# Kernel tuning notes

Measured on AMD Instinct MI355X. Metric: run time of the kernel, lower is better.

Reference implementation:

```python
import jax, jax.numpy as jnp
import numpy as np

DIM = 512; HEADS = 8; DH = 64; CHUNK = 64; DHID = DH * 4; MAX_LR = 1.0; EPS = 1e-6


def rmsnorm(x, w):
    return x * jax.lax.rsqrt(jnp.mean(x * x, axis=-1, keepdims=True) + EPS) * w


def mem_forward(params, x):
    # MemoryMLP(depth=2, expansion=4) wrapped in ResidualNorm
    nw, w0, w1 = params
    h = rmsnorm(x, nw)
    y = jax.nn.gelu(h @ w0) @ w1
    return y + x


def chunk_loss(params, k, lr, v):
    pred = mem_forward(params, k)            # (CHUNK, DH)
    loss = jnp.mean((pred - v) ** 2, axis=-1)  # per-token mse, (CHUNK,)
    return (loss * lr).sum(), loss


def assoc_scan(gates, inputs, prev=None):
    # h_t = g_t * h_{t-1} + x_t along axis=1 (chunks)
    def combine(a, b):
        g1, x1 = a; g2, x2 = b
        return g1 * g2, x2 + g2 * x1
    G, X = jax.lax.associative_scan(combine, (gates, inputs), axis=1)
    if prev is None:
        return X
    return X + G * prev[:, None]


def setup_inputs() -> dict:
    key = jax.random.key(0)
    ks = jax.random.split(key, 8)
    B, N = 2, 4096
    s = 0.02
    return {
        'seq': jax.random.normal(ks[0], (B, N, DIM), jnp.float32),
        'store_norm_w': jnp.ones((DIM,), jnp.float32),
        'Wk': jax.random.normal(ks[1], (DIM, HEADS * DH), jnp.float32) * s,
        'Wv': jax.random.normal(ks[2], (DIM, HEADS * DH), jnp.float32) * s,
        'Wstep': jax.random.normal(ks[3], (DIM, HEADS), jnp.float32) * s,
        'bstep': jnp.zeros((HEADS,), jnp.float32),
        'Wmom': jax.random.normal(ks[4], (DIM, HEADS), jnp.float32) * s,
        'bmom': jnp.zeros((HEADS,), jnp.float32),
        'Wdec': jax.random.normal(ks[5], (DIM, HEADS), jnp.float32) * s,
        'bdec': jnp.zeros((HEADS,), jnp.float32),
        'mem_norm_w': jnp.ones((HEADS, DH), jnp.float32),
        'mem_w0': jax.random.normal(ks[6], (HEADS, DH, DHID), jnp.float32) * s,
        'mem_w1': jax.random.normal(ks[7], (HEADS, DHID, DH), jnp.float32) * s,
    }


def reference(seq, store_norm_w, Wk, Wv, Wstep, bstep, Wmom, bmom, Wdec, bdec, mem_norm_w, mem_w0, mem_w1):
    B, N, _ = seq.shape
    nc = N // CHUNK
    bh = B * HEADS
    x = rmsnorm(seq, store_norm_w)                        # store pre-norm, (B,N,D)
    # per-token adaptive lr: 'b n h -> (b h) n', sigmoid * max_lr
    lr = jax.nn.sigmoid(x @ Wstep + bstep) * MAX_LR       # (B,N,H)
    lr = lr.transpose(0, 2, 1).reshape(bh, nc, CHUNK)
    # chunk-pooled rep (AveragePool) -> momentum / decay gates per chunk
    pooled = x.reshape(B, nc, CHUNK, DIM).mean(axis=2)    # (B,nc,D)
    mom = jax.nn.sigmoid(pooled @ Wmom + bmom).transpose(0, 2, 1).reshape(bh, nc, 1)
    decay = jax.nn.sigmoid(pooled @ Wdec + bdec).transpose(0, 2, 1).reshape(bh, nc, 1)

    def split(t):  # (B,N,H*DH) -> (bh, nc, CHUNK, DH)
        return t.reshape(B, N, HEADS, DH).transpose(0, 2, 1, 3).reshape(bh, nc, CHUNK, DH)
    k = split(x @ Wk)
    v = split(x @ Wv)

    # initial fast weights per (b h) stream: repeat 'h ... -> (b h) ...'
    params0 = (jnp.tile(mem_norm_w, (B, 1)),
               jnp.tile(mem_w0, (B, 1, 1)),
               jnp.tile(mem_w1, (B, 1, 1)))

    # per-chunk per-stream grads via vmap(grad) (all chunks share the initial weights)
    grad_fn = jax.grad(chunk_loss, has_aux=True)
    per_chunk = jax.vmap(grad_fn, in_axes=(None, 0, 0, 0))
    per_bh = jax.vmap(per_chunk, in_axes=(0, 0, 0, 0))
    grads, _ = per_bh(params0, k, lr, v)                  # tuple of (bh, nc, *shape)

    finals = []
    for g, w0 in zip(grads, params0):
        surprise = -g
        extra = (1,) * (g.ndim - 2)
        m = mom.reshape(bh, nc, *extra)
        d = decay.reshape(bh, nc, *extra)
        update = assoc_scan(m, surprise)                  # momentum scan, zero init
        wts = assoc_scan(1.0 - d, update, prev=w0)        # decay recurrence from init weights
        finals.append(wts[:, -1].reshape(bh, -1))
    return jnp.concatenate(finals, axis=-1)              # (bh, DH + DH*DHID + DHID*DH)
```

## Files before the change

kernel.cpp:

```cpp
#include <hip/hip_runtime.h>
#include <math.h>

typedef __attribute__((ext_vector_type(8)))  __bf16 bf16x8;
typedef __attribute__((ext_vector_type(4)))  float  f32x4;
typedef __attribute__((ext_vector_type(4)))  unsigned short ushort4v;
typedef __attribute__((ext_vector_type(8)))  unsigned short ushort8v;

#define MFMA16(acc, a, b) acc = __builtin_amdgcn_mfma_f32_16x16x32_bf16((a),(b),(acc),0,0,0)

__device__ inline unsigned short f2b(float f) {
    __bf16 b = (__bf16)f;
    union { __bf16 b; unsigned short u; } v; v.b = b;
    return v.u;
}
__device__ inline float b2f(unsigned short h) {
    union { unsigned int u; float f; } v; v.u = ((unsigned int)h) << 16;
    return v.f;
}
__device__ inline float fast_rcp(float x) { return __builtin_amdgcn_rcpf(x); }
__device__ inline float tanh_fast(float z) {
    float e = __expf(2.0f * z);
    return 1.0f - 2.0f * fast_rcp(e + 1.0f);
}
__device__ inline float gelu_g(float x) {
    const float c0 = 0.7978845608028654f, c1 = 0.044715f;
    float z = c0 * x * (1.0f + c1 * x * x);
    return 0.5f * x * (1.0f + tanh_fast(z));
}
__device__ inline void gelu_both(float x, float& g, float& gp) {
    const float c0 = 0.7978845608028654f, c1 = 0.044715f;
    float x2 = x * x;
    float z  = c0 * x * (1.0f + c1 * x2);
    float t  = tanh_fast(z);
    g  = 0.5f * x * (1.0f + t);
    float dz = c0 * (1.0f + 3.0f * c1 * x2);
    gp = 0.5f * (1.0f + t) + 0.5f * x * (1.0f - t * t) * dz;
}
__device__ inline float sigmoidf(float x) { return fast_rcp(1.0f + __expf(-x)); }

__global__ __launch_bounds__(256) void k_wprep(
    const float* __restrict__ Wk, const float* __restrict__ Wv,
    const float* __restrict__ w0_g, const float* __restrict__ w1_g,
    const float* __restrict__ nw_g,
    unsigned short* __restrict__ WkvT, unsigned short* __restrict__ w0fT,
    unsigned short* __restrict__ w1T, unsigned short* __restrict__ w0N,
    unsigned short* __restrict__ w1N)
{
    const int bid = blockIdx.x, tid = threadIdx.x;
    __shared__ float tile[64][65];
    if (bid < 128) {
        int kt = bid >> 4, nt = bid & 15;
        const float* src = (nt < 8) ? Wk : Wv;
        int ncol0 = (nt & 7) * 64;
        for (int ii = 0; ii < 16; ++ii) {
            int idx = tid + ii * 256; int r = idx >> 6, cc = idx & 63;
            tile[r][cc] = src[(size_t)(kt * 64 + r) * 512 + ncol0 + cc];
        }
        __syncthreads();
        for (int ii = 0; ii < 16; ++ii) {
            int idx = tid + ii * 256; int r = idx >> 6, cc = idx & 63;
            WkvT[(size_t)(nt * 64 + r) * 512 + kt * 64 + cc] = f2b(tile[cc][r]);
        }
    } else if (bid < 160) {
        int q = bid - 128; int hh = q >> 2, it = q & 3;
        const float* w0h = w0_g + hh * 16384;
        for (int ii = 0; ii < 16; ++ii) {
            int idx = tid + ii * 256; int r = idx >> 6, cc = idx & 63;
            tile[r][cc] = w0h[r * 256 + it * 64 + cc];
        }
        __syncthreads();
        for (int ii = 0; ii < 16; ++ii) {
            int idx = tid + ii * 256; int r = idx >> 6, cc = idx & 63;
            w0fT[hh * 16384 + (it * 64 + r) * 64 + cc] = f2b(nw_g[hh * 64 + cc] * tile[cc][r]);
        }
    } else if (bid < 192) {
        int q = bid - 160; int hh = q >> 2, it = q & 3;
        const float* w1h = w1_g + hh * 16384;
        for (int ii = 0; ii < 16; ++ii) {
            int idx = tid + ii * 256; int r = idx >> 6, cc = idx & 63;
            tile[r][cc] = w1h[(it * 64 + r) * 64 + cc];
        }
        __syncthreads();
        for (int ii = 0; ii < 16; ++ii) {
            int idx = tid + ii * 256; int r = idx >> 6, cc = idx & 63;
            w1T[hh * 16384 + r * 256 + it * 64 + cc] = f2b(tile[cc][r]);
        }
    } else {
        int q = bid - 192;
        int gid = q * 2048 + tid * 8;
        const float* s; unsigned short* d;
        if (gid < 131072) { s = w0_g + gid; d = w0N + gid; }
        else              { s = w1_g + (gid - 131072); d = w1N + (gid - 131072); }
        #pragma unroll
        for (int jj = 0; jj < 8; ++jj) d[jj] = f2b(s[jj]);
    }
}

__global__ __launch_bounds__(256) void k_rms_lr(
    const float* __restrict__ seq, const float* __restrict__ wnorm,
    const float* __restrict__ Wstep, const float* __restrict__ bstep,
    unsigned short* __restrict__ xb, float* __restrict__ lrb)
{
    const int wid = threadIdx.x >> 6, lane = threadIdx.x & 63;
    const int t = blockIdx.x * 4 + wid;
    const float* row = seq + (size_t)t * 512 + lane * 8;
    float v[8];
    *(f32x4*)&v[0] = *(const f32x4*)row;
    *(f32x4*)&v[4] = *(const f32x4*)(row + 4);
    float ss = 0.f;
    #pragma unroll
    for (int j = 0; j < 8; ++j) ss += v[j] * v[j];
    #pragma unroll
    for (int o = 1; o < 64; o <<= 1) ss += __shfl_xor(ss, o);
    float rr = rsqrtf(ss * (1.0f / 512.0f) + 1e-6f);
    const float* wn = wnorm + lane * 8;
    ushort8v xs;
    float acc[8] = {0.f,0.f,0.f,0.f,0.f,0.f,0.f,0.f};
    #pragma unroll
    for (int j = 0; j < 8; ++j) {
        float xf = v[j] * rr * wn[j];
        xs[j] = f2b(xf);
        const float* wrow = Wstep + (size_t)(lane * 8 + j) * 8;
        #pragma unroll
        for (int h = 0; h < 8; ++h) acc[h] = fmaf(xf, wrow[h], acc[h]);
    }
    *(ushort8v*)(xb + (size_t)t * 512 + lane * 8) = xs;
    #pragma unroll
    for (int h = 0; h < 8; ++h) {
        #pragma unroll
        for (int o = 1; o < 64; o <<= 1) acc[h] += __shfl_xor(acc[h], o);
    }
    if (lane == 0) {
        #pragma unroll
        for (int h = 0; h < 8; ++h) lrb[(size_t)t * 8 + h] = sigmoidf(acc[h] + bstep[h]);
    }
}

__global__ __launch_bounds__(256) void k_poolgates(
    const unsigned short* __restrict__ xb,
    const float* __restrict__ Wmom, const float* __restrict__ bmom,
    const float* __restrict__ Wdec, const float* __restrict__ bdec,
    float* __restrict__ momout, float* __restrict__ decout)
{
    __shared__ float sP[4][512];
    __shared__ float pooled[512];
    const int bc = blockIdx.x, tid = threadIdx.x;
    const int q = tid >> 6, lane = tid & 63, d0 = lane * 8;
    float p[8] = {0.f,0.f,0.f,0.f,0.f,0.f,0.f,0.f};
    for (int tt = 0; tt < 16; ++tt) {
        int t = q * 16 + tt;
        ushort8v v = *(const ushort8v*)(xb + (size_t)(bc * 64 + t) * 512 + d0);
        #pragma unroll
        for (int j = 0; j < 8; ++j) p[j] += b2f(v[j]);
    }
    #pragma unroll
    for (int j = 0; j < 8; ++j) sP[q][d0 + j] = p[j];
    __syncthreads();
    #pragma unroll
    for (int half = 0; half < 2; ++half) {
        int d = tid + half * 256;
        pooled[d] = (sP[0][d] + sP[1][d] + sP[2][d] + sP[3][d]) * (1.0f / 64.0f);
    }
    __syncthreads();
    if (tid < 64) {
        const int h = tid & 7, dd0 = tid >> 3;
        float pm = 0.f, pd = 0.f;
        #pragma unroll 8
        for (int it = 0; it < 64; ++it) {
            int d = dd0 + it * 8; float pv = pooled[d];
            pm = fmaf(pv, Wmom[d * 8 + h], pm);
            pd = fmaf(pv, Wdec[d * 8 + h], pd);
        }
        #pragma unroll
        for (int o = 8; o < 64; o <<= 1) { pm += __shfl_xor(pm, o); pd += __shfl_xor(pd, o); }
        if (tid < 8) {
            momout[(size_t)bc * 8 + h] = sigmoidf(pm + bmom[h]);
            decout[(size_t)bc * 8 + h] = sigmoidf(pd + bdec[h]);
        }
    }
}

__global__ __launch_bounds__(256) void k_proj(
    const unsigned short* __restrict__ xb, const unsigned short* __restrict__ WkvT,
    unsigned short* __restrict__ kbh, unsigned short* __restrict__ vb)
{
    __shared__ __attribute__((aligned(16))) unsigned short As[128][72];
    __shared__ __attribute__((aligned(16))) unsigned short Bs[128][72];
    const int tid = threadIdx.x;
    const int bm = blockIdx.x >> 3, bn = blockIdx.x & 7;
    const int m0 = bm * 128, n0 = bn * 128;
    const int wid = tid >> 6, lane = tid & 63, lg = lane >> 4, lo = lane & 15;
    const int wm = wid >> 1, wn = wid & 1;
    f32x4 acc[4][4];
    #pragma unroll
    for (int i = 0; i < 4; ++i)
        #pragma unroll
        for (int j = 0; j < 4; ++j) acc[i][j] = (f32x4)0.f;

    for (int k0 = 0; k0 < 512; k0 += 64) {
        #pragma unroll
        for (int ii = 0; ii < 4; ++ii) {
            int e0 = tid * 32 + ii * 8;
            int r = e0 >> 6, c = e0 & 63;
            *(bf16x8*)&As[r][c] = *(const bf16x8*)(xb   + (size_t)(m0 + r) * 512 + k0 + c);
            *(bf16x8*)&Bs[r][c] = *(const bf16x8*)(WkvT + (size_t)(n0 + r) * 512 + k0 + c);
        }
        __syncthreads();
        #pragma unroll
        for (int ks = 0; ks < 2; ++ks) {
            bf16x8 aF[4], bF[4];
            #pragma unroll
            for (int mt = 0; mt < 4; ++mt) aF[mt] = *(const bf16x8*)&As[wm * 64 + mt * 16 + lo][ks * 32 + 8 * lg];
            #pragma unroll
            for (int nt = 0; nt < 4; ++nt) bF[nt] = *(const bf16x8*)&Bs[wn * 64 + nt * 16 + lo][ks * 32 + 8 * lg];
            #pragma unroll
            for (int mt = 0; mt < 4; ++mt)
                #pragma unroll
                for (int nt = 0; nt < 4; ++nt) MFMA16(acc[mt][nt], aF[mt], bF[nt]);
        }
        __syncthreads();
    }
    #pragma unroll
    for (int mt = 0; mt < 4; ++mt)
        #pragma unroll
        for (int nt = 0; nt < 4; ++nt)
            #pragma unroll
            for (int r = 0; r < 4; ++r) {
                int row = m0 + wm * 64 + mt * 16 + lg * 4 + r;
                int col = n0 + wn * 64 + nt * 16 + lo;
                unsigned short val = f2b(acc[mt][nt][r]);
                if (col < 512) kbh[(size_t)row * 512 + col] = val;
                else           vb[(size_t)row * 512 + col - 512] = val;
            }
}

__global__ void k_coeff(const float* __restrict__ mom, const float* __restrict__ dec,
                        float* __restrict__ coeff, float* __restrict__ Aout)
{
    __shared__ float sm[1024], sd[1024];
    int tid = threadIdx.x;
    #pragma unroll
    for (int i = 0; i < 4; ++i) {
        int idx = (tid + i * 64) * 4;
        *(f32x4*)&sm[idx] = *(const f32x4*)&mom[idx];
        *(f32x4*)&sd[idx] = *(const f32x4*)&dec[idx];
    }
    __syncthreads();
    int s = tid;
    if (s >= 16) return;
    int b = s >> 3, h = s & 7;
    float P = 1.f, S = 1.f;
    coeff[s * 64 + 63] = 1.f;
    for (int cc = 62; cc >= 0; --cc) {
        float Dn = 1.f - sd[(b * 64 + cc + 1) * 8 + h];
        float Mn = sm[(b * 64 + cc + 1) * 8 + h];
        P *= Dn;
        S = P + Mn * S;
        coeff[s * 64 + cc] = S;
    }
    float D0 = 1.f - sd[(b * 64) * 8 + h];
    Aout[s] = P * D0;
}

__global__ __launch_bounds__(256) void k_fwd(
    const unsigned short* __restrict__ kbh, const unsigned short* __restrict__ vb,
    const float* __restrict__ lrb, const float* __restrict__ cfb,
    const unsigned short* __restrict__ w0fT, const unsigned short* __restrict__ w1T,
    unsigned short* __restrict__ uws, unsigned short* __restrict__ ews,
    unsigned short* __restrict__ ewsT)
{
    __shared__ __attribute__((aligned(16))) unsigned short sU[64][72];
    __shared__ __attribute__((aligned(16))) unsigned short sG[2][64][72];
    const int tid = threadIdx.x, blk = blockIdx.x;
    const int s = blk >> 6, c = blk & 63;
    const int b = s >> 3, h = s & 7;
    const int row0 = b * 4096 + c * 64;
    const int wid = tid >> 6, lane = tid & 63, lg = lane >> 4, lo = lane & 15;
    const size_t ubase = (size_t)blk * 4096;

    {
        int r = tid >> 2, c0 = (tid & 3) * 16;
        const unsigned short* kr = kbh + (size_t)(row0 + r) * 512 + h * 64 + c0;
        ushort8v k0 = *(const ushort8v*)kr;
        ushort8v k1 = *(const ushort8v*)(kr + 8);
        float kv[16];
        float ss = 0.f;
        #pragma unroll
        for (int j = 0; j < 8; ++j) { kv[j] = b2f(k0[j]); kv[8 + j] = b2f(k1[j]); }
        #pragma unroll
        for (int j = 0; j < 16; ++j) ss += kv[j] * kv[j];
        ss += __shfl_xor(ss, 1);
        ss += __shfl_xor(ss, 2);
        float rr = rsqrtf(ss * (1.0f / 64.0f) + 1e-6f);
        ushort8v u0, u1;
        #pragma unroll
        for (int j = 0; j < 8; ++j) { u0[j] = f2b(kv[j] * rr); u1[j] = f2b(kv[8 + j] * rr); }
        *(ushort8v*)&sU[r][c0]     = u0;
        *(ushort8v*)&sU[r][c0 + 8] = u1;
        *(ushort8v*)(uws + ubase + r * 64 + c0)     = u0;
        *(ushort8v*)(uws + ubase + r * 64 + c0 + 8) = u1;
    }
    __syncthreads();

    const unsigned short* w0h = w0fT + h * 16384;
    const unsigned short* w1h = w1T  + h * 16384;
    bf16x8 aF0 = *(const bf16x8*)&sU[wid * 16 + lo][8 * lg];
    bf16x8 aF1 = *(const bf16x8*)&sU[wid * 16 + lo][32 + 8 * lg];

    f32x4 yac[4];
    #pragma unroll
    for (int nt = 0; nt < 4; ++nt) yac[nt] = (f32x4)0.f;

    for (int is = 0; is < 4; ++is) {
        const int bi = is & 1;
        f32x4 a1[4];
        #pragma unroll
        for (int nt = 0; nt < 4; ++nt) a1[nt] = (f32x4)0.f;
        #pragma unroll
        for (int nt = 0; nt < 4; ++nt) {
            bf16x8 b0 = *(const bf16x8*)(w0h + (size_t)(is * 64 + nt * 16 + lo) * 64 + 8 * lg);
            bf16x8 b1 = *(const bf16x8*)(w0h + (size_t)(is * 64 + nt * 16 + lo) * 64 + 32 + 8 * lg);
            MFMA16(a1[nt], aF0, b0);
            MFMA16(a1[nt], aF1, b1);
        }
        #pragma unroll
        for (int nt = 0; nt < 4; ++nt)
            #pragma unroll
            for (int r = 0; r < 4; ++r) {
                int t = wid * 16 + lg * 4 + r;
                sG[bi][t][nt * 16 + lo] = f2b(gelu_g(a1[nt][r]));
            }
        __syncthreads();
        #pragma unroll
        for (int ks = 0; ks < 2; ++ks) {
            bf16x8 aW = *(const bf16x8*)(w1h + (size_t)(wid * 16 + lo) * 256 + is * 64 + ks * 32 + 8 * lg);
            #pragma unroll
            for (int nt = 0; nt < 4; ++nt) {
                bf16x8 bG = *(const bf16x8*)&sG[bi][nt * 16 + lo][ks * 32 + 8 * lg];
                MFMA16(yac[nt], aW, bG);
            }
        }
    }

    float coefv = cfb[s * 64 + c];
    ushort4v evs[4];
    #pragma unroll
    for (int nt = 0; nt < 4; ++nt) {
        int t = nt * 16 + lo; int grow = row0 + t;
        float sc = -coefv * lrb[(size_t)grow * 8 + h] * (2.0f / 64.0f);
        ushort4v k4 = *(const ushort4v*)(kbh + (size_t)grow * 512 + h * 64 + wid * 16 + lg * 4);
        ushort4v v4 = *(const ushort4v*)(vb  + (size_t)grow * 512 + h * 64 + wid * 16 + lg * 4);
        ushort4v ev;
        #pragma unroll
        for (int r = 0; r < 4; ++r)
            ev[r] = f2b(sc * (yac[nt][r] + b2f(k4[r]) - b2f(v4[r])));
        evs[nt] = ev;
        *(ushort4v*)(ews + ubase + t * 64 + wid * 16 + lg * 4) = ev;
    }

    #pragma unroll
    for (int nt = 0; nt < 4; ++nt)
        *(ushort4v*)&sG[0][nt * 16 + lo][wid * 16 + lg * 4] = evs[nt];
    __syncthreads();
    {
        int r2 = tid >> 2, c2 = (tid & 3) * 16;
        ushort8v o0, o1;
        #pragma unroll
        for (int jj = 0; jj < 8; ++jj) o0[jj] = sG[0][c2 + jj][r2];
        #pragma unroll
        for (int jj = 0; jj < 8; ++jj) o1[jj] = sG[0][c2 + 8 + jj][r2];
        *(ushort8v*)(ewsT + ubase + r2 * 64 + c2)     = o0;
        *(ushort8v*)(ewsT + ubase + r2 * 64 + c2 + 8) = o1;
    }
}

__global__ __launch_bounds__(256) void k_bwd(
    const unsigned short* __restrict__ uws, const unsigned short* __restrict__ ews,
    const unsigned short* __restrict__ ewsT,
    const unsigned short* __restrict__ w0fT, const unsigned short* __restrict__ w0N,
    const unsigned short* __restrict__ w1N, const float* __restrict__ nw_g,
    float* __restrict__ pws, float* __restrict__ gnwb)
{
    __shared__ __attribute__((aligned(16))) unsigned short sGT[2][64][72];
    __shared__ __attribute__((aligned(16))) unsigned short sDAT[2][64][72];
    __shared__ __attribute__((aligned(16))) unsigned short sDAN[2][64][68];
    const int tid = threadIdx.x, blk = blockIdx.x;
    const int s = blk >> 5, ksl = (blk >> 2) & 7, is = blk & 3;
    const int h = s & 7;
    const int wid = tid >> 6, lane = tid & 63, lg = lane >> 4, lo = lane & 15;

    f32x4 gw1a[4], gw0a[4];
    #pragma unroll
    for (int nt = 0; nt < 4; ++nt) { gw1a[nt] = (f32x4)0.f; gw0a[nt] = (f32x4)0.f; }
    float gnwp[4] = {0.f, 0.f, 0.f, 0.f};

    const unsigned short* w0fh = w0fT + h * 16384;
    const unsigned short* w0nh = w0N  + h * 16384;
    const unsigned short* w1nh = w1N  + h * 16384;

    for (int tt = 0; tt < 8; ++tt) {
        const int bi = tt & 1;
        const int chunk = ksl * 8 + tt;
        const size_t base = (size_t)(s * 64 + chunk) * 4096;

        unsigned short utg[16];
        #pragma unroll
        for (int ks = 0; ks < 2; ++ks)
            #pragma unroll
            for (int jj = 0; jj < 8; ++jj)
                utg[ks * 8 + jj] = uws[base + (size_t)(ks * 32 + 8 * lg + jj) * 64 + wid * 16 + lo];
        ushort4v u4n[4];
        #pragma unroll
        for (int nt = 0; nt < 4; ++nt)
            u4n[nt] = *(const ushort4v*)(uws + base + (size_t)(nt * 16 + lo) * 64 + wid * 16 + lg * 4);

        f32x4 a1[4];
        #pragma unroll
        for (int nt = 0; nt < 4; ++nt) a1[nt] = (f32x4)0.f;
        bf16x8 aF0 = *(const bf16x8*)(uws + base + (size_t)(wid * 16 + lo) * 64 + 8 * lg);
        bf16x8 aF1 = *(const bf16x8*)(uws + base + (size_t)(wid * 16 + lo) * 64 + 32 + 8 * lg);
        #pragma unroll
        for (int nt = 0; nt < 4; ++nt) {
            bf16x8 b0 = *(const bf16x8*)(w0fh + (size_t)(is * 64 + nt * 16 + lo) * 64 + 8 * lg);
            bf16x8 b1 = *(const bf16x8*)(w0fh + (size_t)(is * 64 + nt * 16 + lo) * 64 + 32 + 8 * lg);
            MFMA16(a1[nt], aF0, b0);
            MFMA16(a1[nt], aF1, b1);
        }
        float gpv[4][4];
        #pragma unroll
        for (int nt = 0; nt < 4; ++nt) {
            ushort4v gv;
            #pragma unroll
            for (int r = 0; r < 4; ++r) {
                float g, gp; gelu_both(a1[nt][r], g, gp);
                gv[r] = f2b(g); gpv[nt][r] = gp;
            }
            *(ushort4v*)&sGT[bi][nt * 16 + lo][wid * 16 + lg * 4] = gv;
        }

        f32x4 dga[4];
        #pragma unroll
        for (int nt = 0; nt < 4; ++nt) dga[nt] = (f32x4)0.f;
        bf16x8 eF0 = *(const bf16x8*)(ews + base + (size_t)(wid * 16 + lo) * 64 + 8 * lg);
        bf16x8 eF1 = *(const bf16x8*)(ews + base + (size_t)(wid * 16 + lo) * 64 + 32 + 8 * lg);
        #pragma unroll
        for (int nt = 0; nt < 4; ++nt) {
            bf16x8 b0 = *(const bf16x8*)(w1nh + (size_t)(is * 64 + nt * 16 + lo) * 64 + 8 * lg);
            bf16x8 b1 = *(const bf16x8*)(w1nh + (size_t)(is * 64 + nt * 16 + lo) * 64 + 32 + 8 * lg);
            MFMA16(dga[nt], eF0, b0);
            MFMA16(dga[nt], eF1, b1);
        }
        #pragma unroll
        for (int nt = 0; nt < 4; ++nt) {
            ushort4v dv;
            #pragma unroll
            for (int r = 0; r < 4; ++r) dv[r] = f2b(dga[nt][r] * gpv[nt][r]);
            *(ushort4v*)&sDAT[bi][nt * 16 + lo][wid * 16 + lg * 4] = dv;
            #pragma unroll
            for (int r = 0; r < 4; ++r) sDAN[bi][wid * 16 + lg * 4 + r][nt * 16 + lo] = dv[r];
        }
        __syncthreads();

        #pragma unroll
        for (int ks = 0; ks < 2; ++ks) {
            bf16x8 aG = *(const bf16x8*)&sGT[bi][wid * 16 + lo][ks * 32 + 8 * lg];
            #pragma unroll
            for (int nt = 0; nt < 4; ++nt) {
                bf16x8 bE = *(const bf16x8*)(ewsT + base + (size_t)(nt * 16 + lo) * 64 + ks * 32 + 8 * lg);
                MFMA16(gw1a[nt], aG, bE);
            }
        }
        #pragma unroll
        for (int ks = 0; ks < 2; ++ks) {
            union { ushort8v u; bf16x8 b; } cu;
            #pragma unroll
            for (int jj = 0; jj < 8; ++jj) cu.u[jj] = utg[ks * 8 + jj];
            #pragma unroll
            for (int nt = 0; nt < 4; ++nt) {
                bf16x8 bD = *(const bf16x8*)&sDAT[bi][nt * 16 + lo][ks * 32 + 8 * lg];
                MFMA16(gw0a[nt], cu.b, bD);
            }
        }
        f32x4 dht[4];
        #pragma unroll
        for (int nt = 0; nt < 4; ++nt) dht[nt] = (f32x4)0.f;
        #pragma unroll
        for (int ks = 0; ks < 2; ++ks) {
            bf16x8 aW0 = *(const bf16x8*)(w0nh + (size_t)(wid * 16 + lo) * 256 + is * 64 + ks * 32 + 8 * lg);
            #pragma unroll
            for (int nt = 0; nt < 4; ++nt) {
                bf16x8 bDA = *(const bf16x8*)&sDAN[bi][nt * 16 + lo][ks * 32 + 8 * lg];
                MFMA16(dht[nt], aW0, bDA);
            }
        }
        #pragma unroll
        for (int nt = 0; nt < 4; ++nt)
            #pragma unroll
            for (int r = 0; r < 4; ++r)
                gnwp[r] += b2f(u4n[nt][r]) * dht[nt][r];
    }

    size_t pb = (size_t)blk * 8192;
    #pragma unroll
    for (int nt = 0; nt < 4; ++nt)
        #pragma unroll
        for (int r = 0; r < 4; ++r)
            pws[pb + (size_t)(wid * 16 + lg * 4 + r) * 64 + nt * 16 + lo] = gw1a[nt][r];
    #pragma unroll
    for (int r = 0; r < 4; ++r) {
        float nwv = nw_g[h * 64 + wid * 16 + lg * 4 + r];
        #pragma unroll
        for (int nt = 0; nt < 4; ++nt)
            pws[pb + 4096 + (size_t)(wid * 16 + lg * 4 + r) * 64 + nt * 16 + lo] = nwv * gw0a[nt][r];
    }
    #pragma unroll
    for (int r = 0; r < 4; ++r) {
        #pragma unroll
        for (int o = 1; o < 16; o <<= 1) gnwp[r] += __shfl_xor(gnwp[r], o);
    }
    if (lo == 0) {
        #pragma unroll
        for (int r = 0; r < 4; ++r)
            gnwb[(size_t)blk * 64 + wid * 16 + lg * 4 + r] = gnwp[r];
    }
}

__global__ __launch_bounds__(256) void k_reduce(
    const float* __restrict__ pws, const float* __restrict__ gnwb,
    const float* __restrict__ Ab,
    const float* __restrict__ nw_g, const float* __restrict__ w0_g,
    const float* __restrict__ w1_g, float* __restrict__ out)
{
    int gid = blockIdx.x * 256 + threadIdx.x;
    if (gid >= 16 * 32832) return;
    int s = gid / 32832, r = gid % 32832;
    int h = s & 7;
    float A = Ab[s];
    float val;
    if (r < 64) {
        val = A * nw_g[h * 64 + r];
        #pragma unroll
        for (int ks = 0; ks < 8; ++ks)
            #pragma unroll
            for (int i2 = 0; i2 < 4; ++i2)
                val += gnwb[(size_t)(s * 32 + ks * 4 + i2) * 64 + r];
    } else if (r < 16448) {
        int rr = r - 64; int d = rr >> 8; int i = rr & 255; int i2 = i >> 6, iloc = i & 63;
        val = A * w0_g[h * 16384 + rr];
        #pragma unroll
        for (int ks = 0; ks < 8; ++ks)
            val += pws[(size_t)(s * 32 + ks * 4 + i2) * 8192 + 4096 + d * 64 + iloc];
    } else {
        int rr = r - 16448; int i = rr >> 6; int j = rr & 63; int i2 = i >> 6, iloc = i & 63;
        val = A * w1_g[h * 16384 + rr];
        #pragma unroll
        for (int ks = 0; ks < 8; ++ks)
            val += pws[(size_t)(s * 32 + ks * 4 + i2) * 8192 + iloc * 64 + j];
    }
    out[gid] = val;
}

extern "C" void kernel_launch(void* const* d_in, const int* in_sizes, int n_in,
                              void* d_out, int out_size, void* d_ws, size_t ws_size,
                              hipStream_t stream) {
    (void)in_sizes; (void)n_in; (void)out_size; (void)ws_size;
    const float* seq   = (const float*)d_in[0];
    const float* snw   = (const float*)d_in[1];
    const float* Wk    = (const float*)d_in[2];
    const float* Wv    = (const float*)d_in[3];
    const float* Wstep = (const float*)d_in[4];
    const float* bstep = (const float*)d_in[5];
    const float* Wmom  = (const float*)d_in[6];
    const float* bmom  = (const float*)d_in[7];
    const float* Wdec  = (const float*)d_in[8];
    const float* bdec  = (const float*)d_in[9];
    const float* nw_g  = (const float*)d_in[10];
    const float* w0_g  = (const float*)d_in[11];
    const float* w1_g  = (const float*)d_in[12];
    float* out = (float*)d_out;

    char* ws = (char*)d_ws;
    unsigned short* xb   = (unsigned short*)(ws + 0);
    unsigned short* uws  = (unsigned short*)(ws + 0);
    unsigned short* WkvT = (unsigned short*)(ws + 8388608);
    float*          gnwb = (float*)        (ws + 8388608);
    unsigned short* kbh  = (unsigned short*)(ws + 9437184);
    unsigned short* vb   = (unsigned short*)(ws + 17825792);
    float*          pws  = (float*)        (ws + 9437184);
    unsigned short* ews  = (unsigned short*)(ws + 26214400);
    unsigned short* ewsT = (unsigned short*)(ws + 34603008);
    unsigned short* w0fT = (unsigned short*)(ws + 42991616);
    unsigned short* w1T  = (unsigned short*)(ws + 43253760);
    unsigned short* w0N  = (unsigned short*)(ws + 43515904);
    unsigned short* w1N  = (unsigned short*)(ws + 43778048);
    float* lrb  = (float*)(ws + 44040192);
    float* momb = (float*)(ws + 44302336);
    float* decb = (float*)(ws + 44306432);
    float* cfb  = (float*)(ws + 44310528);
    float* Ab   = (float*)(ws + 44314624);

    k_wprep    <<<320, 256, 0, stream>>>(Wk, Wv, w0_g, w1_g, nw_g, WkvT, w0fT, w1T, w0N, w1N);
    k_rms_lr   <<<2048, 256, 0, stream>>>(seq, snw, Wstep, bstep, xb, lrb);
    k_poolgates<<<128, 256, 0, stream>>>(xb, Wmom, bmom, Wdec, bdec, momb, decb);
    k_proj     <<<512, 256, 0, stream>>>(xb, WkvT, kbh, vb);
    k_coeff    <<<1, 64, 0, stream>>>(momb, decb, cfb, Ab);
    k_fwd      <<<1024, 256, 0, stream>>>(kbh, vb, lrb, cfb, w0fT, w1T, uws, ews, ewsT);
    k_bwd      <<<512, 256, 0, stream>>>(uws, ews, ewsT, w0fT, w0N, w1N, nw_g, pws, gnwb);
    k_reduce   <<<2052, 256, 0, stream>>>(pws, gnwb, Ab, nw_g, w0_g, w1_g, out);
}
```

Measured before the change: 135.4 us.

## Software-pipeline per-chunk global loads in k_bwd across double-buffered iterations

Restructures the k_bwd chunk loop into a 2x-unrolled software pipeline that issues the next chunk's global loads (u, e fragments) before running the current chunk's second-phase MFMAs. The aim is to hide global-memory latency behind compute. In exchange the two register sets raise register pressure, which may lower occupancy. The last iteration redundantly reloads the final chunk to avoid reading past the block's range.

```diff
diff --git a/kernel.cpp b/kernel.cpp
--- a/kernel.cpp
+++ b/kernel.cpp
@@ -374,6 +374,89 @@
     }
 }
 
+#define LOADSET(BASE, UTG, U4N, AF0, AF1, EF0, EF1)                                      \
+    {                                                                                     \
+        _Pragma("unroll")                                                                 \
+        for (int ks = 0; ks < 2; ++ks)                                                    \
+            _Pragma("unroll")                                                             \
+            for (int jj = 0; jj < 8; ++jj)                                                \
+                UTG[ks * 8 + jj] = uws[(BASE) + (size_t)(ks * 32 + 8 * lg + jj) * 64 + wid * 16 + lo]; \
+        _Pragma("unroll")                                                                 \
+        for (int nt = 0; nt < 4; ++nt)                                                    \
+            U4N[nt] = *(const ushort4v*)(uws + (BASE) + (size_t)(nt * 16 + lo) * 64 + wid * 16 + lg * 4); \
+        AF0 = *(const bf16x8*)(uws + (BASE) + (size_t)(wid * 16 + lo) * 64 + 8 * lg);     \
+        AF1 = *(const bf16x8*)(uws + (BASE) + (size_t)(wid * 16 + lo) * 64 + 32 + 8 * lg);\
+        EF0 = *(const bf16x8*)(ews + (BASE) + (size_t)(wid * 16 + lo) * 64 + 8 * lg);     \
+        EF1 = *(const bf16x8*)(ews + (BASE) + (size_t)(wid * 16 + lo) * 64 + 32 + 8 * lg);\
+    }
+
+#define PHASEA(BI, AF0, AF1, EF0, EF1)                                                    \
+    {                                                                                     \
+        f32x4 a1[4];                                                                      \
+        _Pragma("unroll") for (int nt = 0; nt < 4; ++nt) a1[nt] = (f32x4)0.f;             \
+        _Pragma("unroll") for (int nt = 0; nt < 4; ++nt) {                                \
+            bf16x8 b0 = *(const bf16x8*)(w0fh + (size_t)(is * 64 + nt * 16 + lo) * 64 + 8 * lg);      \
+            bf16x8 b1 = *(const bf16x8*)(w0fh + (size_t)(is * 64 + nt * 16 + lo) * 64 + 32 + 8 * lg); \
+            MFMA16(a1[nt], AF0, b0);                                                      \
+            MFMA16(a1[nt], AF1, b1);                                                      \
+        }                                                                                 \
+        float gpv[4][4];                                                                  \
+        _Pragma("unroll") for (int nt = 0; nt < 4; ++nt) {                                \
+            ushort4v gv;                                                                  \
+            _Pragma("unroll") for (int r = 0; r < 4; ++r) {                               \
+                float g, gp; gelu_both(a1[nt][r], g, gp);                                 \
+                gv[r] = f2b(g); gpv[nt][r] = gp;                                          \
+            }                                                                             \
+            *(ushort4v*)&sGT[BI][nt * 16 + lo][wid * 16 + lg * 4] = gv;                   \
+        }                                                                                 \
+        f32x4 dga[4];                                                                     \
+        _Pragma("unroll") for (int nt = 0; nt < 4; ++nt) dga[nt] = (f32x4)0.f;            \
+        _Pragma("unroll") for (int nt = 0; nt < 4; ++nt) {                                \
+            bf16x8 b0 = *(const bf16x8*)(w1nh + (size_t)(is * 64 + nt * 16 + lo) * 64 + 8 * lg);      \
+            bf16x8 b1 = *(const bf16x8*)(w1nh + (size_t)(is * 64 + nt * 16 + lo) * 64 + 32 + 8 * lg); \
+            MFMA16(dga[nt], EF0, b0);                                                     \
+            MFMA16(dga[nt], EF1, b1);                                                     \
+        }                                                                                 \
+        _Pragma("unroll") for (int nt = 0; nt < 4; ++nt) {                                \
+            ushort4v dv;                                                                  \
+            _Pragma("unroll") for (int r = 0; r < 4; ++r) dv[r] = f2b(dga[nt][r] * gpv[nt][r]);       \
+            *(ushort4v*)&sDAT[BI][nt * 16 + lo][wid * 16 + lg * 4] = dv;                  \
+            _Pragma("unroll") for (int r = 0; r < 4; ++r)                                 \
+                sDAN[BI][wid * 16 + lg * 4 + r][nt * 16 + lo] = dv[r];                    \
+        }                                                                                 \
+    }
+
+#define PHASEB(BI, BASE, UTG, U4N)                                                        \
+    {                                                                                     \
+        _Pragma("unroll") for (int ks = 0; ks < 2; ++ks) {                                \
+            bf16x8 aG = *(const bf16x8*)&sGT[BI][wid * 16 + lo][ks * 32 + 8 * lg];        \
+            _Pragma("unroll") for (int nt = 0; nt < 4; ++nt) {                            \
+                bf16x8 bE = *(const bf16x8*)(ewsT + (BASE) + (size_t)(nt * 16 + lo) * 64 + ks * 32 + 8 * lg); \
+                MFMA16(gw1a[nt], aG, bE);                                                 \
+            }                                                                             \
+        }                                                                                 \
+        _Pragma("unroll") for (int ks = 0; ks < 2; ++ks) {                                \
+            union { ushort8v u; bf16x8 b; } cu;                                           \
+            _Pragma("unroll") for (int jj = 0; jj < 8; ++jj) cu.u[jj] = UTG[ks * 8 + jj]; \
+            _Pragma("unroll") for (int nt = 0; nt < 4; ++nt) {                            \
+                bf16x8 bD = *(const bf16x8*)&sDAT[BI][nt * 16 + lo][ks * 32 + 8 * lg];    \
+                MFMA16(gw0a[nt], cu.b, bD);                                               \
+            }                                                                             \
+        }                                                                                 \
+        f32x4 dht[4];                                                                     \
+        _Pragma("unroll") for (int nt = 0; nt < 4; ++nt) dht[nt] = (f32x4)0.f;            \
+        _Pragma("unroll") for (int ks = 0; ks < 2; ++ks) {                                \
+            bf16x8 aW0 = *(const bf16x8*)(w0nh + (size_t)(wid * 16 + lo) * 256 + is * 64 + ks * 32 + 8 * lg); \
+            _Pragma("unroll") for (int nt = 0; nt < 4; ++nt) {                            \
+                bf16x8 bDA = *(const bf16x8*)&sDAN[BI][nt * 16 + lo][ks * 32 + 8 * lg];   \
+                MFMA16(dht[nt], aW0, bDA);                                                \
+            }                                                                             \
+        }                                                                                 \
+        _Pragma("unroll") for (int nt = 0; nt < 4; ++nt)                                  \
+            _Pragma("unroll") for (int r = 0; r < 4; ++r)                                 \
+                gnwp[r] += b2f(U4N[nt][r]) * dht[nt][r];                                  \
+    }
+
 __global__ __launch_bounds__(256) void k_bwd(
     const unsigned short* __restrict__ uws, const unsigned short* __restrict__ ews,
     const unsigned short* __restrict__ ewsT,
@@ -398,106 +481,26 @@
     const unsigned short* w0nh = w0N  + h * 16384;
     const unsigned short* w1nh = w1N  + h * 16384;
 
-    for (int tt = 0; tt < 8; ++tt) {
-        const int bi = tt & 1;
-        const int chunk = ksl * 8 + tt;
-        const size_t base = (size_t)(s * 64 + chunk) * 4096;
-
-        unsigned short utg[16];
-        #pragma unroll
-        for (int ks = 0; ks < 2; ++ks)
-            #pragma unroll
-            for (int jj = 0; jj < 8; ++jj)
-                utg[ks * 8 + jj] = uws[base + (size_t)(ks * 32 + 8 * lg + jj) * 64 + wid * 16 + lo];
-        ushort4v u4n[4];
-        #pragma unroll
-        for (int nt = 0; nt < 4; ++nt)
-            u4n[nt] = *(const ushort4v*)(uws + base + (size_t)(nt * 16 + lo) * 64 + wid * 16 + lg * 4);
-
-        f32x4 a1[4];
-        #pragma unroll
-        for (int nt = 0; nt < 4; ++nt) a1[nt] = (f32x4)0.f;
-        bf16x8 aF0 = *(const bf16x8*)(uws + base + (size_t)(wid * 16 + lo) * 64 + 8 * lg);
-        bf16x8 aF1 = *(const bf16x8*)(uws + base + (size_t)(wid * 16 + lo) * 64 + 32 + 8 * lg);
-        #pragma unroll
-        for (int nt = 0; nt < 4; ++nt) {
-            bf16x8 b0 = *(const bf16x8*)(w0fh + (size_t)(is * 64 + nt * 16 + lo) * 64 + 8 * lg);
-            bf16x8 b1 = *(const bf16x8*)(w0fh + (size_t)(is * 64 + nt * 16 + lo) * 64 + 32 + 8 * lg);
-            MFMA16(a1[nt], aF0, b0);
-            MFMA16(a1[nt], aF1, b1);
-        }
-        float gpv[4][4];
-        #pragma unroll
-        for (int nt = 0; nt < 4; ++nt) {
-            ushort4v gv;
-            #pragma unroll
-            for (int r = 0; r < 4; ++r) {
-                float g, gp; gelu_both(a1[nt][r], g, gp);
-                gv[r] = f2b(g); gpv[nt][r] = gp;
-            }
-            *(ushort4v*)&sGT[bi][nt * 16 + lo][wid * 16 + lg * 4] = gv;
-        }
-
-        f32x4 dga[4];
-        #pragma unroll
-        for (int nt = 0; nt < 4; ++nt) dga[nt] = (f32x4)0.f;
-        bf16x8 eF0 = *(const bf16x8*)(ews + base + (size_t)(wid * 16 + lo) * 64 + 8 * lg);
-        bf16x8 eF1 = *(const bf16x8*)(ews + base + (size_t)(wid * 16 + lo) * 64 + 32 + 8 * lg);
-        #pragma unroll
-        for (int nt = 0; nt < 4; ++nt) {
-            bf16x8 b0 = *(const bf16x8*)(w1nh + (size_t)(is * 64 + nt * 16 + lo) * 64 + 8 * lg);
-            bf16x8 b1 = *(const bf16x8*)(w1nh + (size_t)(is * 64 + nt * 16 + lo) * 64 + 32 + 8 * lg);
-            MFMA16(dga[nt], eF0, b0);
-            MFMA16(dga[nt], eF1, b1);
-        }
-        #pragma unroll
-        for (int nt = 0; nt < 4; ++nt) {
-            ushort4v dv;
-            #pragma unroll
-            for (int r = 0; r < 4; ++r) dv[r] = f2b(dga[nt][r] * gpv[nt][r]);
-            *(ushort4v*)&sDAT[bi][nt * 16 + lo][wid * 16 + lg * 4] = dv;
-            #pragma unroll
-            for (int r = 0; r < 4; ++r) sDAN[bi][wid * 16 + lg * 4 + r][nt * 16 + lo] = dv[r];
-        }
-        __syncthreads();
-
-        #pragma unroll
-        for (int ks = 0; ks < 2; ++ks) {
-            bf16x8 aG = *(const bf16x8*)&sGT[bi][wid * 16 + lo][ks * 32 + 8 * lg];
-            #pragma unroll
-            for (int nt = 0; nt < 4; ++nt) {
-                bf16x8 bE = *(const bf16x8*)(ewsT + base + (size_t)(nt * 16 + lo) * 64 + ks * 32 + 8 * lg);
-                MFMA16(gw1a[nt], aG, bE);
-            }
-        }
-        #pragma unroll
-        for (int ks = 0; ks < 2; ++ks) {
-            union { ushort8v u; bf16x8 b; } cu;
-            #pragma unroll
-            for (int jj = 0; jj < 8; ++jj) cu.u[jj] = utg[ks * 8 + jj];
-            #pragma unroll
-            for (int nt = 0; nt < 4; ++nt) {
-                bf16x8 bD = *(const bf16x8*)&sDAT[bi][nt * 16 + lo][ks * 32 + 8 * lg];
-                MFMA16(gw0a[nt], cu.b, bD);
-            }
-        }
-        f32x4 dht[4];
-        #pragma unroll
-        for (int nt = 0; nt < 4; ++nt) dht[nt] = (f32x4)0.f;
-        #pragma unroll
-        for (int ks = 0; ks < 2; ++ks) {
-            bf16x8 aW0 = *(const bf16x8*)(w0nh + (size_t)(wid * 16 + lo) * 256 + is * 64 + ks * 32 + 8 * lg);
-            #pragma unroll
-            for (int nt = 0; nt < 4; ++nt) {
-                bf16x8 bDA = *(const bf16x8*)&sDAN[bi][nt * 16 + lo][ks * 32 + 8 * lg];
-                MFMA16(dht[nt], aW0, bDA);
-            }
-        }
-        #pragma unroll
-        for (int nt = 0; nt < 4; ++nt)
-            #pragma unroll
-            for (int r = 0; r < 4; ++r)
-                gnwp[r] += b2f(u4n[nt][r]) * dht[nt][r];
+    unsigned short utgA[16], utgB[16];
+    ushort4v u4nA[4], u4nB[4];
+    bf16x8 aF0A, aF1A, eF0A, eF1A, aF0B, aF1B, eF0B, eF1B;
+    const size_t sbase = (size_t)(s * 64 + ksl * 8) * 4096;
+    LOADSET(sbase, utgA, u4nA, aF0A, aF1A, eF0A, eF1A);
+
+    for (int t2 = 0; t2 < 4; ++t2) {
+        const size_t base0 = sbase + (size_t)(t2 * 2) * 4096;
+        const size_t base1 = base0 + 4096;
+        const size_t base2 = (t2 < 3) ? (base1 + 4096) : base1;
+
+        PHASEA(0, aF0A, aF1A, eF0A, eF1A);
+        __syncthreads();
+        LOADSET(base1, utgB, u4nB, aF0B, aF1B, eF0B, eF1B);
+        PHASEB(0, base0, utgA, u4nA);
+
+        PHASEA(1, aF0B, aF1B, eF0B, eF1B);
+        __syncthreads();
+        LOADSET(base2, utgA, u4nA, aF0A, aF1A, eF0A, eF1A);
+        PHASEB(1, base1, utgB, u4nB);
     }
 
     size_t pb = (size_t)blk * 8192;
```

Measured after the change: 148.1 us. 9.4% more time.
